# Performance work log

Measured on AMD Instinct MI355X. Metric: run time of the kernel, lower is better.

## Reference

```python
import jax, jax.numpy as jnp
import numpy as np

B, L, D, U = 8, 512, 256, 32

def setup_inputs() -> dict:
    key = jax.random.key(0)
    ks = jax.random.split(key, 6)
    g = lambda k, shape: jax.random.normal(k, shape, dtype=jnp.float32) * (2.0 / sum(shape)) ** 0.5
    return {
        "x": jax.random.normal(ks[0], (B, L, D), dtype=jnp.float32),
        "Wt": g(ks[1], (D, U)),
        "Wx": g(ks[2], (D, U)),
        "bh": jnp.zeros((U,), dtype=jnp.float32),
        "Wa": g(ks[3], (U, 1)),
        "ba": jnp.zeros((1,), dtype=jnp.float32),
    }

def reference(x, Wt, Wx, bh, Wa, ba):
    # q: [B,L,1,U], k: [B,1,L,U]
    q = jnp.einsum('bld,du->blu', x, Wt)[:, :, None, :]
    k = jnp.einsum('bld,du->blu', x, Wx)[:, None, :, :]
    beta = jnp.tanh(q + k + bh)                      # [B,L,L,U]
    alpha = jnp.einsum('bstu,u->bst', beta, Wa[:, 0]) + ba[0]  # [B,L,L]
    a = jax.nn.softmax(alpha, axis=-1)               # softmax over keys
    c_r = jnp.einsum('bst,btd->bsd', a, x)           # [B,L,D]
    return c_r
```

## Files before the change

### kernel.cpp

```cpp
#include <hip/hip_runtime.h>

#define B 8
#define L 512
#define D 256
#define U 32
#define ST 16
#define QKR 8

#define K2E    2.885390081777927f
#define KLOG2E 1.4426950408889634f

typedef __attribute__((ext_vector_type(8))) _Float16 half8;
typedef __attribute__((ext_vector_type(4))) float    float4v;

__global__ __launch_bounds__(256) void qk_kernel(
    const float* __restrict__ x,
    const float* __restrict__ Wt,
    const float* __restrict__ Wx,
    const float* __restrict__ bh,
    float* __restrict__ qb,
    float* __restrict__ kk,
    _Float16* __restrict__ xT)
{
    __shared__ float  xs[QKR][D + 1];
    __shared__ float4 pq[3][QKR][8];
    __shared__ float4 pk[3][QKR][8];

    const int b    = blockIdx.x & 7;
    const int tile = blockIdx.x >> 3;
    const int row0 = b * L + tile * QKR;
    const int tid  = threadIdx.x;

    const float4* xg = (const float4*)(x + row0 * D);
    #pragma unroll
    for (int i = tid; i < QKR * D / 4; i += 256) {
        float4 v = xg[i];
        int r = i >> 6;
        int c = (i & 63) << 2;
        xs[r][c] = v.x; xs[r][c + 1] = v.y; xs[r][c + 2] = v.z; xs[r][c + 3] = v.w;
    }
    __syncthreads();

    {
        const int d = tid;
        half8 h;
        #pragma unroll
        for (int r = 0; r < QKR; ++r) h[r] = (_Float16)xs[r][d];
        *(half8*)(xT + (b * D + d) * L + tile * QKR) = h;
    }

    const int dq = tid >> 6;
    const int r  = (tid >> 3) & 7;
    const int g  = tid & 7;
    const float4* __restrict__ Wt4 = (const float4*)Wt;
    const float4* __restrict__ Wx4 = (const float4*)Wx;

    float4 qa = {0.f, 0.f, 0.f, 0.f};
    float4 ka = {0.f, 0.f, 0.f, 0.f};
    const int d0 = dq * (D / 4);
    #pragma unroll 8
    for (int dd = 0; dd < D / 4; ++dd) {
        const int d = d0 + dd;
        float  xv = xs[r][d];
        float4 wt = Wt4[d * 8 + g];
        float4 wx = Wx4[d * 8 + g];
        qa.x = fmaf(xv, wt.x, qa.x); qa.y = fmaf(xv, wt.y, qa.y);
        qa.z = fmaf(xv, wt.z, qa.z); qa.w = fmaf(xv, wt.w, qa.w);
        ka.x = fmaf(xv, wx.x, ka.x); ka.y = fmaf(xv, wx.y, ka.y);
        ka.z = fmaf(xv, wx.z, ka.z); ka.w = fmaf(xv, wx.w, ka.w);
    }

    if (dq > 0) { pq[dq - 1][r][g] = qa; pk[dq - 1][r][g] = ka; }
    __syncthreads();
    if (dq == 0) {
        #pragma unroll
        for (int w = 0; w < 3; ++w) {
            float4 a = pq[w][r][g], c = pk[w][r][g];
            qa.x += a.x; qa.y += a.y; qa.z += a.z; qa.w += a.w;
            ka.x += c.x; ka.y += c.y; ka.z += c.z; ka.w += c.w;
        }
        float4 b4 = ((const float4*)bh)[g];
        qa.x += b4.x; qa.y += b4.y; qa.z += b4.z; qa.w += b4.w;
        const int row = row0 + r;
        ((float4*)qb)[row * 8 + g] = qa;
        ((float4*)kk)[row * 8 + g] = ka;
    }
}

__global__ __launch_bounds__(1024) void attn_kernel(
    const _Float16* __restrict__ xT,
    const float* __restrict__ qb,
    const float* __restrict__ kk,
    const float* __restrict__ Wa,
    const float* __restrict__ ba,
    float* __restrict__ out)
{
    const int blk = blockIdx.x;
    const int b   = blk & 7;
    const int s0  = (blk >> 3) * ST;
    const int tid = threadIdx.x;
    const int wv  = tid >> 6;
    const int ln  = tid & 63;
    const int t   = tid & 511;
    const int sh  = tid >> 9;
    const int wl  = wv & 7;

    __shared__ _Float16 a_sh[ST][L + 8];
    __shared__ float redm[ST][8];
    __shared__ float reds[ST][8];
    __shared__ float inv_sh[ST];

    float kv[U];
    {
        const float4* k4 = (const float4*)(kk + (b * L + t) * U);
        #pragma unroll
        for (int c = 0; c < 8; ++c) {
            float4 v = k4[c];
            kv[4*c]   = v.x * K2E; kv[4*c+1] = v.y * K2E;
            kv[4*c+2] = v.z * K2E; kv[4*c+3] = v.w * K2E;
        }
    }
    float sWa = 0.f;
    #pragma unroll
    for (int u = 0; u < U; ++u) sWa += Wa[u];
    const float base = (sWa + ba[0]) * KLOG2E;

    const float* __restrict__ qrow = qb + (b * L + s0 + sh * 8) * U;
    float avK[8];
    #pragma unroll 1
    for (int s = 0; s < 8; ++s) {
        const float* __restrict__ q = qrow + s * U;
        float tacc = 0.f;
        #pragma unroll
        for (int u = 0; u < U; ++u) {
            float z = fmaf(q[u], K2E, kv[u]);
            float e = __builtin_amdgcn_exp2f(z);
            float r = __builtin_amdgcn_rcpf(e + 1.f);
            tacc = fmaf(r, Wa[u], tacc);
        }
        avK[s] = fmaf(tacc, -2.f * KLOG2E, base);
    }

    #pragma unroll
    for (int s = 0; s < 8; ++s) {
        float v = avK[s];
        #pragma unroll
        for (int off = 1; off < 64; off <<= 1) v = fmaxf(v, __shfl_xor(v, off));
        if (ln == 0) redm[sh * 8 + s][wl] = v;
    }
    __syncthreads();
    float e2[8];
    #pragma unroll
    for (int s = 0; s < 8; ++s) {
        float gm = redm[sh * 8 + s][0];
        #pragma unroll
        for (int w = 1; w < 8; ++w) gm = fmaxf(gm, redm[sh * 8 + s][w]);
        float e = __builtin_amdgcn_exp2f(avK[s] - gm + 10.f);
        e2[s] = e;
        float ss = e;
        #pragma unroll
        for (int off = 1; off < 64; off <<= 1) ss += __shfl_xor(ss, off);
        if (ln == 0) reds[sh * 8 + s][wl] = ss;
    }
    __syncthreads();
    if (tid < ST) {
        float ss = 0.f;
        #pragma unroll
        for (int w = 0; w < 8; ++w) ss += reds[tid][w];
        inv_sh[tid] = __builtin_amdgcn_rcpf(ss);
    }
    #pragma unroll
    for (int s = 0; s < 8; ++s)
        a_sh[sh * 8 + s][t] = (_Float16)e2[s];
    __syncthreads();

    const int n0   = wv * 16;
    const int row  = ln & 15;
    const int quad = ln >> 4;
    const _Float16* __restrict__ xrow = xT + (b * D + n0 + row) * L + quad * 8;
    const _Float16* __restrict__ arow = &a_sh[row][quad * 8];

    float4v acc = {0.f, 0.f, 0.f, 0.f};
    #pragma unroll 4
    for (int kc = 0; kc < 16; ++kc) {
        half8 af = *(const half8*)(arow + kc * 32);
        half8 bf = *(const half8*)(xrow + kc * 32);
        acc = __builtin_amdgcn_mfma_f32_16x16x32_f16(af, bf, acc, 0, 0, 0);
    }

    #pragma unroll
    for (int r = 0; r < 4; ++r) {
        const int m = quad * 4 + r;
        out[(b * L + s0 + m) * D + n0 + row] = acc[r] * inv_sh[m];
    }
}

extern "C" void kernel_launch(void* const* d_in, const int* in_sizes, int n_in,
                              void* d_out, int out_size, void* d_ws, size_t ws_size,
                              hipStream_t stream)
{
    const float* x  = (const float*)d_in[0];
    const float* Wt = (const float*)d_in[1];
    const float* Wx = (const float*)d_in[2];
    const float* bh = (const float*)d_in[3];
    const float* Wa = (const float*)d_in[4];
    const float* ba = (const float*)d_in[5];
    float* out = (float*)d_out;

    float*    qb = (float*)d_ws;
    float*    kk = qb + B * L * U;
    _Float16* xT = (_Float16*)(kk + B * L * U);

    qk_kernel<<<B * L / QKR, 256, 0, stream>>>(x, Wt, Wx, bh, qb, kk, xT);
    attn_kernel<<<B * (L / ST), 1024, 0, stream>>>(xT, qb, kk, Wa, ba, out);
}
```

Baseline: 117.8 us.

## Factor tanh exponent into per-row exp products and drop softmax max pass

Precomputes exp(2q+2bh) and exp(2k) in the projection kernel, so the L×L×U inner loop needs a multiply and reciprocal instead of an exp per element. It also removes the max-subtraction reduction of the softmax: exponentials are written straight to shared memory as fp16 and summed afterwards, which cuts one barrier and one reduction pass. The risk is overflow or infinity when q+k is large (the product of two exps can overflow fp32), and fp16 overflow or underflow of unnormalized softmax weights, since the logits are no longer shifted by their maximum.

```diff
diff --git a/kernel.cpp b/kernel.cpp
--- a/kernel.cpp
+++ b/kernel.cpp
@@ -18,8 +18,8 @@
     const float* __restrict__ Wt,
     const float* __restrict__ Wx,
     const float* __restrict__ bh,
-    float* __restrict__ qb,
-    float* __restrict__ kk,
+    float* __restrict__ Eq,
+    float* __restrict__ Ek,
     _Float16* __restrict__ xT)
 {
     __shared__ float  xs[QKR][D + 1];
@@ -80,17 +80,24 @@
             ka.x += c.x; ka.y += c.y; ka.z += c.z; ka.w += c.w;
         }
         float4 b4 = ((const float4*)bh)[g];
-        qa.x += b4.x; qa.y += b4.y; qa.z += b4.z; qa.w += b4.w;
+        qa.x = __builtin_amdgcn_exp2f((qa.x + b4.x) * K2E);
+        qa.y = __builtin_amdgcn_exp2f((qa.y + b4.y) * K2E);
+        qa.z = __builtin_amdgcn_exp2f((qa.z + b4.z) * K2E);
+        qa.w = __builtin_amdgcn_exp2f((qa.w + b4.w) * K2E);
+        ka.x = __builtin_amdgcn_exp2f(ka.x * K2E);
+        ka.y = __builtin_amdgcn_exp2f(ka.y * K2E);
+        ka.z = __builtin_amdgcn_exp2f(ka.z * K2E);
+        ka.w = __builtin_amdgcn_exp2f(ka.w * K2E);
         const int row = row0 + r;
-        ((float4*)qb)[row * 8 + g] = qa;
-        ((float4*)kk)[row * 8 + g] = ka;
+        ((float4*)Eq)[row * 8 + g] = qa;
+        ((float4*)Ek)[row * 8 + g] = ka;
     }
 }
 
 __global__ __launch_bounds__(1024) void attn_kernel(
     const _Float16* __restrict__ xT,
-    const float* __restrict__ qb,
-    const float* __restrict__ kk,
+    const float* __restrict__ Eq,
+    const float* __restrict__ Ek,
     const float* __restrict__ Wa,
     const float* __restrict__ ba,
     float* __restrict__ out)
@@ -103,21 +110,17 @@
     const int ln  = tid & 63;
     const int t   = tid & 511;
     const int sh  = tid >> 9;
-    const int wl  = wv & 7;
 
     __shared__ _Float16 a_sh[ST][L + 8];
-    __shared__ float redm[ST][8];
-    __shared__ float reds[ST][8];
     __shared__ float inv_sh[ST];
 
-    float kv[U];
+    float ek[U];
     {
-        const float4* k4 = (const float4*)(kk + (b * L + t) * U);
+        const float4* k4 = (const float4*)(Ek + (b * L + t) * U);
         #pragma unroll
         for (int c = 0; c < 8; ++c) {
             float4 v = k4[c];
-            kv[4*c]   = v.x * K2E; kv[4*c+1] = v.y * K2E;
-            kv[4*c+2] = v.z * K2E; kv[4*c+3] = v.w * K2E;
+            ek[4*c] = v.x; ek[4*c+1] = v.y; ek[4*c+2] = v.z; ek[4*c+3] = v.w;
         }
     }
     float sWa = 0.f;
@@ -125,53 +128,31 @@
     for (int u = 0; u < U; ++u) sWa += Wa[u];
     const float base = (sWa + ba[0]) * KLOG2E;
 
-    const float* __restrict__ qrow = qb + (b * L + s0 + sh * 8) * U;
-    float avK[8];
+    const float* __restrict__ eqrow = Eq + (b * L + s0 + sh * 8) * U;
     #pragma unroll 1
     for (int s = 0; s < 8; ++s) {
-        const float* __restrict__ q = qrow + s * U;
-        float tacc = 0.f;
+        const float* __restrict__ q = eqrow + s * U;
+        float acc = 0.f;
         #pragma unroll
         for (int u = 0; u < U; ++u) {
-            float z = fmaf(q[u], K2E, kv[u]);
-            float e = __builtin_amdgcn_exp2f(z);
-            float r = __builtin_amdgcn_rcpf(e + 1.f);
-            tacc = fmaf(r, Wa[u], tacc);
+            float E = q[u] * ek[u];
+            float r = __builtin_amdgcn_rcpf(E + 1.f);
+            acc = fmaf(r, Wa[u], acc);
         }
-        avK[s] = fmaf(tacc, -2.f * KLOG2E, base);
-    }
-
-    #pragma unroll
-    for (int s = 0; s < 8; ++s) {
-        float v = avK[s];
-        #pragma unroll
-        for (int off = 1; off < 64; off <<= 1) v = fmaxf(v, __shfl_xor(v, off));
-        if (ln == 0) redm[sh * 8 + s][wl] = v;
+        float avK = fmaf(acc, -2.f * KLOG2E, base);
+        a_sh[sh * 8 + s][t] = (_Float16)__builtin_amdgcn_exp2f(avK);
     }
     __syncthreads();
-    float e2[8];
-    #pragma unroll
-    for (int s = 0; s < 8; ++s) {
-        float gm = redm[sh * 8 + s][0];
+
+    {
+        half8 h = *(const half8*)&a_sh[wv][ln * 8];
+        float ss = 0.f;
         #pragma unroll
-        for (int w = 1; w < 8; ++w) gm = fmaxf(gm, redm[sh * 8 + s][w]);
-        float e = __builtin_amdgcn_exp2f(avK[s] - gm + 10.f);
-        e2[s] = e;
-        float ss = e;
+        for (int i = 0; i < 8; ++i) ss += (float)h[i];
         #pragma unroll
         for (int off = 1; off < 64; off <<= 1) ss += __shfl_xor(ss, off);
-        if (ln == 0) reds[sh * 8 + s][wl] = ss;
+        if (ln == 0) inv_sh[wv] = __builtin_amdgcn_rcpf(ss);
     }
-    __syncthreads();
-    if (tid < ST) {
-        float ss = 0.f;
-        #pragma unroll
-        for (int w = 0; w < 8; ++w) ss += reds[tid][w];
-        inv_sh[tid] = __builtin_amdgcn_rcpf(ss);
-    }
-    #pragma unroll
-    for (int s = 0; s < 8; ++s)
-        a_sh[sh * 8 + s][t] = (_Float16)e2[s];
     __syncthreads();
 
     const int n0   = wv * 16;
@@ -207,10 +188,10 @@
     const float* ba = (const float*)d_in[5];
     float* out = (float*)d_out;
 
-    float*    qb = (float*)d_ws;
-    float*    kk = qb + B * L * U;
-    _Float16* xT = (_Float16*)(kk + B * L * U);
+    float*    Eq = (float*)d_ws;
+    float*    Ek = Eq + B * L * U;
+    _Float16* xT = (_Float16*)(Ek + B * L * U);
 
-    qk_kernel<<<B * L / QKR, 256, 0, stream>>>(x, Wt, Wx, bh, qb, kk, xT);
-    attn_kernel<<<B * (L / ST), 1024, 0, stream>>>(xT, qb, kk, Wa, ba, out);
+    qk_kernel<<<B * L / QKR, 256, 0, stream>>>(x, Wt, Wx, bh, Eq, Ek, xT);
+    attn_kernel<<<B * (L / ST), 1024, 0, stream>>>(xT, Eq, Ek, Wa, ba, out);
 }
```

Result: faster. 108.5 us (-7.9%).
